# Performance work log

Measured on AMD Instinct MI355X. Metric: run time of the kernel, lower is better.

Reference implementation:

```python
import jax, jax.numpy as jnp
import numpy as np

B, C, H, W = 2, 256, 64, 64
NUM_HEADS = 8


def setup_inputs() -> dict:
    key = jax.random.key(0)
    k1, k2, k3 = jax.random.split(key, 3)
    x = jax.random.normal(k1, (B, C, H, W), dtype=jnp.float32)
    # 1x1 convs, bias=False -> plain [out_ch, in_ch] matrices
    w_qkv = jax.random.normal(k2, (3 * C, C), dtype=jnp.float32) * (1.0 / np.sqrt(C))
    w_proj = jax.random.normal(k3, (C, C), dtype=jnp.float32) * (1.0 / np.sqrt(C))
    return {"x": x, "w_qkv": w_qkv, "w_proj": w_proj}


def reference(x, w_qkv, w_proj):
    b, c, h, w = x.shape
    hd = NUM_HEADS
    d = c // hd  # head dim
    n = h * w    # number of tokens

    # 1x1 conv == channel matmul: [3C, C] x [B, C, H, W] -> [B, 3C, H, W]
    qkv = jnp.einsum('oc,bchw->bohw', w_qkv, x)
    q, k, v = jnp.split(qkv, 3, axis=1)

    def reshape(t):
        return t.reshape(b, hd, d, n)  # [B, h, d, N]

    q, k, v = map(reshape, (q, k, v))

    # scores[b,h,i,j] = sum_d q[b,h,d,i] * k[b,h,d,j] / sqrt(d)
    scores = jnp.einsum('bhdi,bhdj->bhij', q, k) / jnp.sqrt(jnp.asarray(d, x.dtype))
    attn = jax.nn.softmax(scores, axis=-1)

    # out[b,h,d,i] = sum_j attn[b,h,i,j] * v[b,h,d,j]
    out = jnp.einsum('bhij,bhdj->bhdi', attn, v)
    out = out.reshape(b, c, h, w)

    return jnp.einsum('oc,bchw->bohw', w_proj, out) + x
```

## Files before the change

### kernel.cpp

```cpp
#include <hip/hip_runtime.h>
#include <hip/hip_bf16.h>

#define NB  2
#define CC  256
#define NHD 8
#define HD  32
#define NT  4096

typedef __bf16 bf16x8 __attribute__((ext_vector_type(8)));
typedef bf16x8 bf16x8_ma __attribute__((may_alias));
typedef __bf16 bf16x4 __attribute__((ext_vector_type(4)));
typedef bf16x4 bf16x4_ma __attribute__((may_alias));
typedef float  f32x4  __attribute__((ext_vector_type(4)));
typedef f32x4  f32x4_ma __attribute__((may_alias));
typedef float  f32x16 __attribute__((ext_vector_type(16)));
typedef unsigned int u32x4 __attribute__((ext_vector_type(4)));
typedef unsigned short u16x8 __attribute__((ext_vector_type(8)));

static __device__ __forceinline__ f32x4 zero4() {
    f32x4 z = {0.f, 0.f, 0.f, 0.f}; return z;
}
static __device__ __forceinline__ f32x16 zero16() {
    f32x16 z = {0.f,0.f,0.f,0.f,0.f,0.f,0.f,0.f,
                0.f,0.f,0.f,0.f,0.f,0.f,0.f,0.f};
    return z;
}

#define QSCALE 0.25505392421795654f

#define CVT_PK(dst, lo, hi_) \
    asm("v_cvt_pk_bf16_f32 %0, %1, %2" : "=v"(dst) : "v"(lo), "v"(hi_))
#define PLSWAP(x, y) \
    asm("v_permlane32_swap_b32 %0, %1" : "+v"(x), "+v"(y))


__global__ __launch_bounds__(256) void convw_k(const float* __restrict__ s1,
                                               __bf16* __restrict__ d1, int n1,
                                               const float* __restrict__ s2,
                                               __bf16* __restrict__ d2, int n2) {
    const int i = blockIdx.x * 256 + threadIdx.x;
    if (i < n1) d1[i] = (__bf16)s1[i];
    else if (i - n1 < n2) d2[i - n1] = (__bf16)s2[i - n1];
}

__global__ __launch_bounds__(256) void qkv_k(const __bf16* __restrict__ wqkv,
                                             const float* __restrict__ x,
                                             __bf16* __restrict__ qt,
                                             __bf16* __restrict__ kt,
                                             __bf16* __restrict__ vv) {
    __shared__ __align__(16) __bf16 T[64][264];

    const int tid  = threadIdx.x;
    const int lane = tid & 63, wv = tid >> 6;
    const int g = lane >> 4, c16 = lane & 15;
    const int b     = blockIdx.z;
    const int obase = blockIdx.y * 192;
    const int tok0  = blockIdx.x * 64;

    const int tok4 = (tid & 15) * 4;
    const int crow = tid >> 4;

#define QKV_EPI(o0p, accv) do {                                                         \
    const int reg = (o0p) >> 8;                                                         \
    const int oo0 = ((o0p) & 255) + g * 4;                                              \
    const int h   = oo0 >> 5;                                                           \
    const int dd0 = oo0 & 31;                                                           \
    const size_t bh = (size_t)(b * NHD + h);                                            \
    _Pragma("unroll")                                                                   \
    for (int js = 0; js < 4; ++js) {                                                    \
        const int tok = tok0 + js * 16 + c16;                                           \
        if (reg == 0) {                                                                 \
            bf16x4 pk;                                                                  \
            _Pragma("unroll")                                                           \
            for (int r = 0; r < 4; ++r) pk[r] = (__bf16)(accv[js][r] * QSCALE);         \
            *(bf16x4_ma*)(qt + (bh * NT + tok) * HD + dd0) = pk;                        \
        } else if (reg == 1) {                                                          \
            bf16x4 pk;                                                                  \
            _Pragma("unroll")                                                           \
            for (int r = 0; r < 4; ++r) pk[r] = (__bf16)accv[js][r];                    \
            *(bf16x4_ma*)(kt + (bh * NT + tok) * HD + dd0) = pk;                        \
        } else {                                                                        \
            _Pragma("unroll")                                                           \
            for (int r = 0; r < 4; ++r)                                                 \
                vv[(bh * HD + dd0 + r) * NT + tok] = (__bf16)accv[js][r];               \
        }                                                                               \
    }                                                                                   \
} while (0)

    {
#pragma unroll
        for (int i = 0; i < 8; ++i) {
            const int c = i * 16 + crow;
            f32x4 v = *(const f32x4_ma*)&x[((size_t)(b * CC + c)) * NT + tok0 + tok4];
#pragma unroll
            for (int j = 0; j < 4; ++j) T[tok4 + j][c] = (__bf16)v[j];
        }
    }

    f32x4 v1[8];
#pragma unroll
    for (int i = 0; i < 8; ++i) {
        const int c = 128 + i * 16 + crow;
        v1[i] = *(const f32x4_ma*)&x[((size_t)(b * CC + c)) * NT + tok0 + tok4];
    }

    const __bf16* arow0 = wqkv + (size_t)(obase + wv * 16 + c16) * CC + g * 8;
    bf16x8 a[8];
#pragma unroll
    for (int kc = 0; kc < 8; ++kc) a[kc] = *(const bf16x8_ma*)(arow0 + kc * 32);

    __syncthreads();

    f32x4 acc[4];
#pragma unroll
    for (int i = 0; i < 4; ++i) acc[i] = zero4();

#pragma unroll
    for (int kc = 0; kc < 4; ++kc) {
#pragma unroll
        for (int js = 0; js < 4; ++js) {
            bf16x8 bb = *(const bf16x8_ma*)&T[js * 16 + c16][kc * 32 + g * 8];
            acc[js] = __builtin_amdgcn_mfma_f32_16x16x32_bf16(a[kc], bb, acc[js], 0, 0, 0);
        }
    }

#pragma unroll
    for (int i = 0; i < 8; ++i) {
        const int c = 128 + i * 16 + crow;
#pragma unroll
        for (int j = 0; j < 4; ++j) T[tok4 + j][c] = (__bf16)v1[i][j];
    }
    __syncthreads();

#pragma unroll
    for (int kc = 4; kc < 8; ++kc) {
#pragma unroll
        for (int js = 0; js < 4; ++js) {
            bf16x8 bb = *(const bf16x8_ma*)&T[js * 16 + c16][kc * 32 + g * 8];
            acc[js] = __builtin_amdgcn_mfma_f32_16x16x32_bf16(a[kc], bb, acc[js], 0, 0, 0);
        }
    }
    QKV_EPI(obase + wv * 16, acc);

#pragma unroll 1
    for (int pass = 1; pass < 3; ++pass) {
        const int o0p = obase + pass * 64 + wv * 16;
        const __bf16* arow = wqkv + (size_t)(o0p + c16) * CC + g * 8;
#pragma unroll
        for (int kc = 0; kc < 8; ++kc) a[kc] = *(const bf16x8_ma*)(arow + kc * 32);
#pragma unroll
        for (int i = 0; i < 4; ++i) acc[i] = zero4();
#pragma unroll
        for (int kc = 0; kc < 8; ++kc) {
#pragma unroll
            for (int js = 0; js < 4; ++js) {
                bf16x8 bb = *(const bf16x8_ma*)&T[js * 16 + c16][kc * 32 + g * 8];
                acc[js] = __builtin_amdgcn_mfma_f32_16x16x32_bf16(a[kc], bb, acc[js], 0, 0, 0);
            }
        }
        QKV_EPI(o0p, acc);
    }
#undef QKV_EPI
}

__global__ __launch_bounds__(256, 4) void attn_k(const __bf16* __restrict__ qt,
                                                 const __bf16* __restrict__ kt,
                                                 const __bf16* __restrict__ vv,
                                                 __bf16* __restrict__ ao,
                                                 float* __restrict__ PO,
                                                 float* __restrict__ PL) {
    __shared__ __align__(16) __bf16 KF[2][4][2][512];
    __shared__ __align__(16) __bf16 VF[2][4][2][512];

    const int tid  = threadIdx.x;
    const int lane = tid & 63, wv = tid >> 6;
    const int c32 = lane & 31, hi = lane >> 5;
    const int bh = blockIdx.y;
    const int b = bh >> 3, h = bh & 7;
    const int seg = blockIdx.z, nseg = gridDim.z;
    const int i0q = blockIdx.x * 128 + wv * 32;

    const __bf16* qbase = qt + ((size_t)bh * NT + i0q) * HD;
    const __bf16* kbase = kt + (size_t)bh * NT * HD;
    const __bf16* vbase = vv + (size_t)bh * HD * NT;

    bf16x8 aq0 = *(const bf16x8_ma*)(qbase + (size_t)c32 * HD + hi * 8);
    bf16x8 aq1 = *(const bf16x8_ma*)(qbase + (size_t)c32 * HD + 16 + hi * 8);

    u16x8 ones_u = {0x3F80,0x3F80,0x3F80,0x3F80,0x3F80,0x3F80,0x3F80,0x3F80};
    const bf16x8 ones = __builtin_bit_cast(bf16x8, ones_u);

    f32x16 oacc = zero16();
    f32x16 lacc = zero16();

#define STAGE(bf, jb) do {                                                              \
    const __bf16* gk = kbase + (size_t)((jb) + wv * 32 + c32) * HD + hi * 8;            \
    __builtin_amdgcn_global_load_lds(                                                   \
        (const __attribute__((address_space(1))) void*)gk,                              \
        (__attribute__((address_space(3))) void*)&KF[bf][wv][0][0],                     \
        16, 0, 0);                                                                      \
    __builtin_amdgcn_global_load_lds(                                                   \
        (const __attribute__((address_space(1))) void*)(gk + 16),                       \
        (__attribute__((address_space(3))) void*)&KF[bf][wv][1][0],                     \
        16, 0, 0);                                                                      \
    const __bf16* gv = vbase + (size_t)c32 * NT + (jb) + wv * 32 + hi * 8;              \
    __builtin_amdgcn_global_load_lds(                                                   \
        (const __attribute__((address_space(1))) void*)gv,                              \
        (__attribute__((address_space(3))) void*)&VF[bf][wv][0][0],                     \
        16, 0, 0);                                                                      \
    __builtin_amdgcn_global_load_lds(                                                   \
        (const __attribute__((address_space(1))) void*)(gv + 16),                       \
        (__attribute__((address_space(3))) void*)&VF[bf][wv][1][0],                     \
        16, 0, 0);                                                                      \
} while (0)

#define SUBTILE(bf, js) do {                                                            \
    bf16x8 fk0 = *(const bf16x8_ma*)&KF[bf][js][0][lane * 8];                           \
    bf16x8 fk1 = *(const bf16x8_ma*)&KF[bf][js][1][lane * 8];                           \
    bf16x8 fv0 = *(const bf16x8_ma*)&VF[bf][js][0][lane * 8];                           \
    bf16x8 fv1 = *(const bf16x8_ma*)&VF[bf][js][1][lane * 8];                           \
    f32x16 s = __builtin_amdgcn_mfma_f32_32x32x16_bf16(fk0, aq0, zero16(), 0, 0, 0);    \
    s = __builtin_amdgcn_mfma_f32_32x32x16_bf16(fk1, aq1, s, 0, 0, 0);                  \
    float p[16];                                                                        \
    _Pragma("unroll")                                                                   \
    for (int r = 0; r < 16; ++r) p[r] = __builtin_amdgcn_exp2f(s[r]);                   \
    unsigned pk[8];                                                                     \
    _Pragma("unroll")                                                                   \
    for (int i = 0; i < 8; ++i) CVT_PK(pk[i], p[2 * i], p[2 * i + 1]);                  \
    PLSWAP(pk[0], pk[2]);                                                               \
    PLSWAP(pk[1], pk[3]);                                                               \
    PLSWAP(pk[4], pk[6]);                                                               \
    PLSWAP(pk[5], pk[7]);                                                               \
    u32x4 a0 = {pk[0], pk[1], pk[2], pk[3]};                                            \
    u32x4 a1 = {pk[4], pk[5], pk[6], pk[7]};                                            \
    const bf16x8 ap0 = __builtin_bit_cast(bf16x8, a0);                                  \
    const bf16x8 ap1 = __builtin_bit_cast(bf16x8, a1);                                  \
    oacc = __builtin_amdgcn_mfma_f32_32x32x16_bf16(ap0, fv0, oacc, 0, 0, 0);            \
    oacc = __builtin_amdgcn_mfma_f32_32x32x16_bf16(ap1, fv1, oacc, 0, 0, 0);            \
    lacc = __builtin_amdgcn_mfma_f32_32x32x16_bf16(ap0, ones, lacc, 0, 0, 0);           \
    lacc = __builtin_amdgcn_mfma_f32_32x32x16_bf16(ap1, ones, lacc, 0, 0, 0);           \
} while (0)

    const int ntiles  = (NT / 128) / nseg;
    const int j_begin = seg * ntiles * 128;

    STAGE(0, j_begin);
    asm volatile("s_waitcnt vmcnt(0)" ::: "memory");
    __syncthreads();

    int buf = 0;
#pragma unroll 1
    for (int t = 0; t < ntiles; ++t) {
        if (t + 1 < ntiles) STAGE(buf ^ 1, j_begin + (t + 1) * 128);
        SUBTILE(buf, 0);
        SUBTILE(buf, 1);
        SUBTILE(buf, 2);
        SUBTILE(buf, 3);
        asm volatile("s_waitcnt vmcnt(0)" ::: "memory");
        __syncthreads();
        buf ^= 1;
    }

#undef STAGE
#undef SUBTILE

    if (nseg == 1) {
#pragma unroll
        for (int g4 = 0; g4 < 4; ++g4) {
#pragma unroll
            for (int r = 0; r < 4; ++r) {
                const int q = 8 * g4 + 4 * hi + r;
                ao[((size_t)(b * NT) + i0q + q) * CC + h * HD + c32] =
                    (__bf16)(oacc[4 * g4 + r] / lacc[4 * g4 + r]);
            }
        }
    } else {
        float* po = PO + (((size_t)seg * NB * NHD + bh) * NT + i0q) * HD;
#pragma unroll
        for (int g4 = 0; g4 < 4; ++g4) {
#pragma unroll
            for (int r = 0; r < 4; ++r) {
                const int q = 8 * g4 + 4 * hi + r;
                po[(size_t)q * HD + c32] = oacc[4 * g4 + r];
            }
        }
        if (c32 == 0) {
            float* pl = PL + ((size_t)seg * NB * NHD + bh) * NT + i0q;
#pragma unroll
            for (int g4 = 0; g4 < 4; ++g4)
#pragma unroll
                for (int r = 0; r < 4; ++r)
                    pl[8 * g4 + 4 * hi + r] = lacc[4 * g4 + r];
        }
    }
}

__global__ __launch_bounds__(256) void comb_k(const float* __restrict__ PO,
                                              const float* __restrict__ PL,
                                              __bf16* __restrict__ ao,
                                              int nseg) {
    const int i = blockIdx.x * 256 + threadIdx.x;
    const int bh = i >> 15;
    const int rem = i & 32767;
    const int n = rem >> 3, g = rem & 7;
    const int b = bh >> 3, h = bh & 7;

    const size_t SEGO = (size_t)(NB * NHD) * NT * HD;
    const size_t SEGL = (size_t)(NB * NHD) * NT;
    const size_t o0i = (((size_t)bh) * NT + n) * HD + g * 4;
    const size_t li  = (size_t)bh * NT + n;

    f32x4 o = *(const f32x4_ma*)&PO[o0i];
    float l = PL[li];
#pragma unroll 3
    for (int s = 1; s < nseg; ++s) {
        o += *(const f32x4_ma*)&PO[(size_t)s * SEGO + o0i];
        l += PL[(size_t)s * SEGL + li];
    }

    bf16x4 pk;
#pragma unroll
    for (int r = 0; r < 4; ++r) pk[r] = (__bf16)(o[r] / l);
    *(bf16x4_ma*)&ao[((size_t)(b * NT) + n) * CC + h * HD + g * 4] = pk;
}

__global__ __launch_bounds__(256) void proj_k(const __bf16* __restrict__ wp,
                                              const __bf16* __restrict__ ao,
                                              const float* __restrict__ x,
                                              float* __restrict__ out) {
    __shared__ __align__(16) __bf16 BF[4][8][512];

    const int lane = threadIdx.x & 63, wv = threadIdx.x >> 6;
    const int g = lane >> 4, c16 = lane & 15;
    const int b    = blockIdx.z;
    const int o0   = blockIdx.y * 64 + wv * 16;
    const int tok0 = blockIdx.x * 64;

    const __bf16* bsrc = ao + ((size_t)(b * NT + tok0 + wv * 16 + c16)) * CC + g * 8;
#pragma unroll
    for (int kc = 0; kc < 4; ++kc) {
        __builtin_amdgcn_global_load_lds(
            (const __attribute__((address_space(1))) void*)(bsrc + kc * 32),
            (__attribute__((address_space(3))) void*)&BF[wv][kc][0],
            16, 0, 0);
    }

    const __bf16* arow = wp + (size_t)(o0 + c16) * CC + g * 8;
    bf16x8 a[8];
#pragma unroll
    for (int kc = 0; kc < 8; ++kc) a[kc] = *(const bf16x8_ma*)(arow + kc * 32);

    float xres[4][4];
#pragma unroll
    for (int js = 0; js < 4; ++js) {
        const int tok = tok0 + js * 16 + c16;
#pragma unroll
        for (int r = 0; r < 4; ++r) {
            const int o = o0 + g * 4 + r;
            xres[js][r] = x[((size_t)(b * CC + o)) * NT + tok];
        }
    }

    __syncthreads();

#pragma unroll
    for (int kc = 4; kc < 8; ++kc) {
        __builtin_amdgcn_global_load_lds(
            (const __attribute__((address_space(1))) void*)(bsrc + kc * 32),
            (__attribute__((address_space(3))) void*)&BF[wv][kc][0],
            16, 0, 0);
    }

    f32x4 acc[4];
#pragma unroll
    for (int i = 0; i < 4; ++i) acc[i] = zero4();

#pragma unroll
    for (int kc = 0; kc < 4; ++kc) {
#pragma unroll
        for (int js = 0; js < 4; ++js) {
            bf16x8 bb = *(const bf16x8_ma*)&BF[js][kc][lane * 8];
            acc[js] = __builtin_amdgcn_mfma_f32_16x16x32_bf16(a[kc], bb, acc[js], 0, 0, 0);
        }
    }

    asm volatile("s_waitcnt vmcnt(0)" ::: "memory");
    __syncthreads();

#pragma unroll
    for (int kc = 4; kc < 8; ++kc) {
#pragma unroll
        for (int js = 0; js < 4; ++js) {
            bf16x8 bb = *(const bf16x8_ma*)&BF[js][kc][lane * 8];
            acc[js] = __builtin_amdgcn_mfma_f32_16x16x32_bf16(a[kc], bb, acc[js], 0, 0, 0);
        }
    }

#pragma unroll
    for (int js = 0; js < 4; ++js) {
        const int tok = tok0 + js * 16 + c16;
#pragma unroll
        for (int r = 0; r < 4; ++r) {
            const int o = o0 + g * 4 + r;
            const size_t idx = ((size_t)(b * CC + o)) * NT + tok;
            out[idx] = acc[js][r] + xres[js][r];
        }
    }
}

extern "C" void kernel_launch(void* const* d_in, const int* in_sizes, int n_in,
                              void* d_out, int out_size, void* d_ws, size_t ws_size,
                              hipStream_t stream) {
    const int SX  = NB * CC * NT;
    const int SW3 = 3 * CC * CC;
    const int SW1 = CC * CC;
    const size_t E = (size_t)SX;

    const float* x  = nullptr;
    const float* wq = nullptr;
    const float* wp = nullptr;
    for (int i = 0; i < n_in; ++i) {
        const int sz = in_sizes[i];
        if (sz == SX || sz == 2 * SX || sz == 4 * SX)           x  = (const float*)d_in[i];
        else if (sz == SW3 || sz == 2 * SW3 || sz == 4 * SW3)   wq = (const float*)d_in[i];
        else if (sz == SW1 || sz == 2 * SW1 || sz == 4 * SW1)   wp = (const float*)d_in[i];
    }
    if (!x || !wq || !wp) {
        x  = (const float*)d_in[0];
        wq = (const float*)d_in[1];
        wp = (const float*)d_in[2];
    }

    __bf16* ws  = (__bf16*)d_ws;
    __bf16* wqb = ws;
    __bf16* wpb = wqb + SW3;
    __bf16* ao  = wpb + SW1;
    __bf16* qt  = ao + E;
    __bf16* kt  = qt + E;
    __bf16* vv  = kt + E;

    const size_t baseB = (size_t)(SW3 + SW1) * 2 + 4 * E * 2;
    const size_t segoB = (size_t)NB * NHD * NT * HD * 4;
    const size_t seglB = (size_t)NB * NHD * NT * 4;
    const int jseg = (ws_size >= baseB + 2 * (segoB + seglB)) ? 2 : 1;
    float* PO = (float*)((char*)d_ws + baseB);
    float* PL = (float*)((char*)d_ws + baseB + (size_t)jseg * segoB);

    float* out = (float*)d_out;

    convw_k<<<dim3((SW3 + SW1 + 255) / 256), 256, 0, stream>>>(wq, wqb, SW3, wp, wpb, SW1);
    qkv_k<<<dim3(NT / 64, 4, NB), 256, 0, stream>>>(wqb, x, qt, kt, vv);
    attn_k<<<dim3(NT / 128, NB * NHD, jseg), 256, 0, stream>>>(qt, kt, vv, ao, PO, PL);
    if (jseg > 1)
        comb_k<<<dim3((NB * NHD * NT * (HD / 4)) / 256), 256, 0, stream>>>(PO, PL, ao, jseg);
    proj_k<<<dim3(NT / 64, CC / 64, NB), 256, 0, stream>>>(wpb, ao, x, out);
}
```

Before: 136.1 us.

## Fuse weight bf16 conversion into GEMM kernels and widen proj tile

Removes the separate weight-conversion kernel launch; qkv_k and proj_k now load fp32 weights and convert them to bf16 in registers. proj_k covers 128 output channels per block, reusing the attention-output tile staged in LDS for a second 64-channel pass, which halves the proj grid. This saves one launch and the workspace round trip for converted weights. In exchange every block re-reads and re-converts fp32 weights, doubling weight load traffic, and proj has fewer blocks.

```diff
diff --git a/kernel.cpp b/kernel.cpp
--- a/kernel.cpp
+++ b/kernel.cpp
@@ -25,6 +25,14 @@
                 0.f,0.f,0.f,0.f,0.f,0.f,0.f,0.f};
     return z;
 }
+static __device__ __forceinline__ bf16x8 ldcvt8(const float* __restrict__ p) {
+    f32x4 lo = *(const f32x4_ma*)p;
+    f32x4 hi = *(const f32x4_ma*)(p + 4);
+    bf16x8 r;
+#pragma unroll
+    for (int i = 0; i < 4; ++i) { r[i] = (__bf16)lo[i]; r[4 + i] = (__bf16)hi[i]; }
+    return r;
+}
 
 #define QSCALE 0.25505392421795654f
 
@@ -34,16 +42,7 @@
     asm("v_permlane32_swap_b32 %0, %1" : "+v"(x), "+v"(y))
 
 
-__global__ __launch_bounds__(256) void convw_k(const float* __restrict__ s1,
-                                               __bf16* __restrict__ d1, int n1,
-                                               const float* __restrict__ s2,
-                                               __bf16* __restrict__ d2, int n2) {
-    const int i = blockIdx.x * 256 + threadIdx.x;
-    if (i < n1) d1[i] = (__bf16)s1[i];
-    else if (i - n1 < n2) d2[i - n1] = (__bf16)s2[i - n1];
-}
-
-__global__ __launch_bounds__(256) void qkv_k(const __bf16* __restrict__ wqkv,
+__global__ __launch_bounds__(256) void qkv_k(const float* __restrict__ wqkv,
                                              const float* __restrict__ x,
                                              __bf16* __restrict__ qt,
                                              __bf16* __restrict__ kt,
@@ -104,10 +103,10 @@
         v1[i] = *(const f32x4_ma*)&x[((size_t)(b * CC + c)) * NT + tok0 + tok4];
     }
 
-    const __bf16* arow0 = wqkv + (size_t)(obase + wv * 16 + c16) * CC + g * 8;
+    const float* arow0 = wqkv + (size_t)(obase + wv * 16 + c16) * CC + g * 8;
     bf16x8 a[8];
 #pragma unroll
-    for (int kc = 0; kc < 8; ++kc) a[kc] = *(const bf16x8_ma*)(arow0 + kc * 32);
+    for (int kc = 0; kc < 8; ++kc) a[kc] = ldcvt8(arow0 + kc * 32);
 
     __syncthreads();
 
@@ -145,9 +144,9 @@
 #pragma unroll 1
     for (int pass = 1; pass < 3; ++pass) {
         const int o0p = obase + pass * 64 + wv * 16;
-        const __bf16* arow = wqkv + (size_t)(o0p + c16) * CC + g * 8;
-#pragma unroll
-        for (int kc = 0; kc < 8; ++kc) a[kc] = *(const bf16x8_ma*)(arow + kc * 32);
+        const float* arow = wqkv + (size_t)(o0p + c16) * CC + g * 8;
+#pragma unroll
+        for (int kc = 0; kc < 8; ++kc) a[kc] = ldcvt8(arow + kc * 32);
 #pragma unroll
         for (int i = 0; i < 4; ++i) acc[i] = zero4();
 #pragma unroll
@@ -324,7 +323,7 @@
     *(bf16x4_ma*)&ao[((size_t)(b * NT) + n) * CC + h * HD + g * 4] = pk;
 }
 
-__global__ __launch_bounds__(256) void proj_k(const __bf16* __restrict__ wp,
+__global__ __launch_bounds__(256) void proj_k(const float* __restrict__ wp,
                                               const __bf16* __restrict__ ao,
                                               const float* __restrict__ x,
                                               float* __restrict__ out) {
@@ -332,9 +331,9 @@
 
     const int lane = threadIdx.x & 63, wv = threadIdx.x >> 6;
     const int g = lane >> 4, c16 = lane & 15;
-    const int b    = blockIdx.z;
-    const int o0   = blockIdx.y * 64 + wv * 16;
-    const int tok0 = blockIdx.x * 64;
+    const int b     = blockIdx.z;
+    const int obase = blockIdx.y * 128;
+    const int tok0  = blockIdx.x * 64;
 
     const __bf16* bsrc = ao + ((size_t)(b * NT + tok0 + wv * 16 + c16)) * CC + g * 8;
 #pragma unroll
@@ -345,20 +344,19 @@
             16, 0, 0);
     }
 
-    const __bf16* arow = wp + (size_t)(o0 + c16) * CC + g * 8;
+    const int o00 = obase + wv * 16;
+    const float* arow = wp + (size_t)(o00 + c16) * CC + g * 8;
     bf16x8 a[8];
 #pragma unroll
-    for (int kc = 0; kc < 8; ++kc) a[kc] = *(const bf16x8_ma*)(arow + kc * 32);
+    for (int kc = 0; kc < 8; ++kc) a[kc] = ldcvt8(arow + kc * 32);
 
     float xres[4][4];
 #pragma unroll
     for (int js = 0; js < 4; ++js) {
         const int tok = tok0 + js * 16 + c16;
 #pragma unroll
-        for (int r = 0; r < 4; ++r) {
-            const int o = o0 + g * 4 + r;
-            xres[js][r] = x[((size_t)(b * CC + o)) * NT + tok];
-        }
+        for (int r = 0; r < 4; ++r)
+            xres[js][r] = x[((size_t)(b * CC + o00 + g * 4 + r)) * NT + tok];
     }
 
     __syncthreads();
@@ -401,9 +399,41 @@
         const int tok = tok0 + js * 16 + c16;
 #pragma unroll
         for (int r = 0; r < 4; ++r) {
-            const int o = o0 + g * 4 + r;
-            const size_t idx = ((size_t)(b * CC + o)) * NT + tok;
+            const size_t idx = ((size_t)(b * CC + o00 + g * 4 + r)) * NT + tok;
             out[idx] = acc[js][r] + xres[js][r];
+        }
+    }
+
+    {
+        const int o01 = obase + 64 + wv * 16;
+        const float* arow1 = wp + (size_t)(o01 + c16) * CC + g * 8;
+#pragma unroll
+        for (int kc = 0; kc < 8; ++kc) a[kc] = ldcvt8(arow1 + kc * 32);
+#pragma unroll
+        for (int js = 0; js < 4; ++js) {
+            const int tok = tok0 + js * 16 + c16;
+#pragma unroll
+            for (int r = 0; r < 4; ++r)
+                xres[js][r] = x[((size_t)(b * CC + o01 + g * 4 + r)) * NT + tok];
+        }
+#pragma unroll
+        for (int i = 0; i < 4; ++i) acc[i] = zero4();
+#pragma unroll
+        for (int kc = 0; kc < 8; ++kc) {
+#pragma unroll
+            for (int js = 0; js < 4; ++js) {
+                bf16x8 bb = *(const bf16x8_ma*)&BF[js][kc][lane * 8];
+                acc[js] = __builtin_amdgcn_mfma_f32_16x16x32_bf16(a[kc], bb, acc[js], 0, 0, 0);
+            }
+        }
+#pragma unroll
+        for (int js = 0; js < 4; ++js) {
+            const int tok = tok0 + js * 16 + c16;
+#pragma unroll
+            for (int r = 0; r < 4; ++r) {
+                const size_t idx = ((size_t)(b * CC + o01 + g * 4 + r)) * NT + tok;
+                out[idx] = acc[js][r] + xres[js][r];
+            }
         }
     }
 }
@@ -432,14 +462,12 @@
     }
 
     __bf16* ws  = (__bf16*)d_ws;
-    __bf16* wqb = ws;
-    __bf16* wpb = wqb + SW3;
-    __bf16* ao  = wpb + SW1;
+    __bf16* ao  = ws;
     __bf16* qt  = ao + E;
     __bf16* kt  = qt + E;
     __bf16* vv  = kt + E;
 
-    const size_t baseB = (size_t)(SW3 + SW1) * 2 + 4 * E * 2;
+    const size_t baseB = 4 * E * 2;
     const size_t segoB = (size_t)NB * NHD * NT * HD * 4;
     const size_t seglB = (size_t)NB * NHD * NT * 4;
     const int jseg = (ws_size >= baseB + 2 * (segoB + seglB)) ? 2 : 1;
@@ -448,10 +476,9 @@
 
     float* out = (float*)d_out;
 
-    convw_k<<<dim3((SW3 + SW1 + 255) / 256), 256, 0, stream>>>(wq, wqb, SW3, wp, wpb, SW1);
-    qkv_k<<<dim3(NT / 64, 4, NB), 256, 0, stream>>>(wqb, x, qt, kt, vv);
+    qkv_k<<<dim3(NT / 64, 4, NB), 256, 0, stream>>>(wq, x, qt, kt, vv);
     attn_k<<<dim3(NT / 128, NB * NHD, jseg), 256, 0, stream>>>(qt, kt, vv, ao, PO, PL);
     if (jseg > 1)
         comb_k<<<dim3((NB * NHD * NT * (HD / 4)) / 256), 256, 0, stream>>>(PO, PL, ao, jseg);
-    proj_k<<<dim3(NT / 64, CC / 64, NB), 256, 0, stream>>>(wpb, ao, x, out);
-}
+    proj_k<<<dim3(NT / 64, 2, NB), 256, 0, stream>>>(wp, ao, x, out);
+}
```

Result: slower. 139.8 us (+2.7%).
